# Optimization experiments

Measured on AMD Instinct MI355X. Metric: run time of the kernel, lower is better.

## Reference

```python
import jax, jax.numpy as jnp
import numpy as np

D = 4096; K = 512; HOP = 512; WIN = 16384
NUM_REGIONS = 1 + (WIN - D) // HOP            # 25
D2_Y = 128; K2 = 128; STRIDE_Y = 2
D3_X = 25; K3 = 256
NR2Y = 1 + (K - D2_Y) // STRIDE_Y             # 193
NR3X = 1 + (NUM_REGIONS - D3_X)               # 1
M = 128


def create_filters(d=D, k=K, sr=44100, start_freq=50, end_freq=6000):
    x = jnp.linspace(0.0, 2 * np.pi, d + 1)[:d]
    num_cycles = start_freq * d / sr
    scaling_ind = np.log(end_freq / start_freq) / k
    window_mask = 1.0 - jnp.cos(x)
    phases = jnp.exp(jnp.arange(float(k)) * scaling_ind)[None, :] * num_cycles * x[:, None]
    filters = jnp.stack((jnp.cos(phases), jnp.sin(phases)), axis=2) * window_mask[:, None, None]
    return filters.astype(jnp.float32)          # [d, k, 2]


def setup_inputs() -> dict:
    key = jax.random.key(0)
    k1, k2, k3, k4 = jax.random.split(key, 4)
    x = jax.random.normal(k1, (128, WIN), dtype=jnp.float32)
    filters = create_filters().reshape(D, 2 * K)                     # [4096, 1024]
    # Conv weights in OIHW layout (torch Conv2d convention), kaiming-ish scale
    conv1_w = jax.random.normal(k2, (K2, 1, 1, D2_Y), dtype=jnp.float32) / np.sqrt(D2_Y)
    conv2_w = jax.random.normal(k3, (K3, K2, D3_X, 1), dtype=jnp.float32) / np.sqrt(K2 * D3_X)
    beta_w = jax.random.normal(k4, (M, NR3X * NR2Y * K3), dtype=jnp.float32) / np.sqrt(NR3X * NR2Y * K3)
    return {"x": x, "filters": filters, "conv1_w": conv1_w, "conv2_w": conv2_w, "beta_w": beta_w}


def reference(x, filters, conv1_w, conv2_w, beta_w):
    B = x.shape[0]
    # unfold(1, D, HOP): overlapping windows -> [B, NUM_REGIONS, D]
    idx = jnp.arange(NUM_REGIONS)[:, None] * HOP + jnp.arange(D)[None, :]
    windows = x[:, idx]                                               # [B, 25, 4096]
    spec = windows @ filters                                          # [B, 25, 1024]
    # complex magnitude^2: pairs of (cos, sin) components
    zx = jnp.sum(spec.reshape(B, NUM_REGIONS, K, 2) ** 2, axis=3)     # [B, 25, 512]
    zx = jnp.log(zx + 1e-14)[:, None]                                 # [B, 1, 25, 512]
    dn = ("NCHW", "OIHW", "NCHW")
    h = jax.lax.conv_general_dilated(zx, conv1_w, (1, STRIDE_Y), "VALID", dimension_numbers=dn)
    h = jax.nn.relu(h)                                                # [B, 128, 25, 193]
    h = jax.lax.conv_general_dilated(h, conv2_w, (1, 1), "VALID", dimension_numbers=dn)
    h = jax.nn.relu(h)                                                # [B, 256, 1, 193]
    y = h.reshape(B, -1) @ beta_w.T                                   # [B, 128]
    return y
```

## Files before the change

### kernel.cpp

```cpp
#include <hip/hip_runtime.h>
#include <hip/hip_bf16.h>
#include <math.h>


typedef __attribute__((ext_vector_type(8))) short s8v;
typedef __attribute__((ext_vector_type(8))) _Float16 half8;
typedef __attribute__((ext_vector_type(16))) float f16v;

__device__ inline ushort f2bf(float f) {
    union { float f; unsigned u; } v; v.f = f;
    unsigned u = v.u;
    return (ushort)((u + 0x7FFFu + ((u >> 16) & 1u)) >> 16);
}

#define K0_E0 2097152
#define K0_E1 2621440
#define K0_E2 2637824
#define K0_E3 3457024
#define K0_E4 9781248
__global__ __launch_bounds__(256)
void k0all(const float* __restrict__ x, const float* __restrict__ filt,
           const float* __restrict__ w1, const float* __restrict__ w2,
           const float* __restrict__ beta,
           _Float16* __restrict__ xh, _Float16* __restrict__ fB,
           ushort* __restrict__ w1b, ushort* __restrict__ w2c,
           ushort* __restrict__ bb) {
    for (int i = blockIdx.x * 256 + threadIdx.x; i < K0_E4; i += gridDim.x * 256) {
        if (i < K0_E0) {
            xh[i] = (_Float16)x[i];
        } else if (i < K0_E1) {
            int o = i - K0_E0;
            int kc8 = o >> 10, nn = o & 1023;
            const float* fp = filt + (size_t)(kc8 * 8) * 1024 + nn;
            half8 v;
#pragma unroll
            for (int j = 0; j < 8; j++) v[j] = (_Float16)fp[(size_t)j * 1024];
            *(half8*)(fB + (size_t)o * 8) = v;
        } else if (i < K0_E2) {
            int o = i - K0_E1;
            w1b[o] = f2bf(w1[o]);
        } else if (i < K0_E3) {
            int o = i - K0_E2;
            int k2 = o & 127;
            int dx = (o >> 7) % 25;
            int k3 = o / 3200;
            w2c[o] = f2bf(w2[(k3 * 128 + k2) * 25 + dx]);
        } else {
            int o = i - K0_E3;
            bb[o] = f2bf(beta[o]);
        }
    }
}

#define K1P(KB, LP, VU, VL, RL, RW, DOPREF, DOWRITE)                               \
  {                                                                                \
    asm volatile("s_waitcnt lgkmcnt(0)" ::: "memory");                             \
    __builtin_amdgcn_s_barrier();                                                  \
    asm volatile("" ::: "memory");                                                 \
    if (DOPREF) {                                                                  \
      RL[0] = *(const half8*)(apt + ((KB) + 2) * 32);                              \
      RL[1] = *(const half8*)(apt + ((KB) + 2) * 32 + 16);                         \
      _Pragma("unroll")                                                            \
      for (int s = 0; s < 2; s++) {                                                \
        const _Float16* pBk = pB + ((size_t)((KB) + 2) * 2 + s) * 16384;           \
        VL[s][0] = *(const half8*)(pBk);                                           \
        VL[s][1] = *(const half8*)(pBk + 256);                                     \
      }                                                                            \
    }                                                                              \
    _Pragma("unroll")                                                              \
    for (int s = 0; s < 2; s++) {                                                  \
      half8 a0 = *(const half8*)((const char*)Al + (LP) * 8192 + s * 4096 +        \
                                 (wm + ml) * 32 + qf * 16);                        \
      half8 a1 = *(const half8*)((const char*)Al + (LP) * 8192 + s * 4096 +        \
                                 (wm + 32 + ml) * 32 + qf * 16);                   \
      acc[0][0] = __builtin_amdgcn_mfma_f32_32x32x16_f16(a0, VU[s][0], acc[0][0], 0, 0, 0); \
      acc[0][1] = __builtin_amdgcn_mfma_f32_32x32x16_f16(a0, VU[s][1], acc[0][1], 0, 0, 0); \
      acc[1][0] = __builtin_amdgcn_mfma_f32_32x32x16_f16(a1, VU[s][0], acc[1][0], 0, 0, 0); \
      acc[1][1] = __builtin_amdgcn_mfma_f32_32x32x16_f16(a1, VU[s][1], acc[1][1], 0, 0, 0); \
    }                                                                              \
    if (DOWRITE) {                                                                 \
      half8* dnx = (half8*)((char*)Al + (1 - (LP)) * 8192);                        \
      dnx[t] = RW[0];                                                              \
      dnx[256 + t] = RW[1];                                                        \
    }                                                                              \
  }

__global__ __launch_bounds__(256)
void k1_mfma(const _Float16* __restrict__ xh, const _Float16* __restrict__ fB,
             ushort* __restrict__ zxb) {
    __shared__ _Float16 Al[2][4096];
    const int t  = threadIdx.x;
    const int n0 = blockIdx.y * 128;
    const int m0 = blockIdx.x * 128;
    const int w  = t >> 6, l = t & 63;
    const int wm = (w >> 1) * 64, wn = (w & 1) * 64;
    const int qf = l >> 5;
    const int ml = l & 31;

    const int srow = t >> 1;
    const int sq   = t & 1;
    const int gm   = m0 + srow;
    const _Float16* apt = xh + (gm / 25) * 16384 + (gm % 25) * 512 + sq * 8;

    const _Float16* pB = fB + ((size_t)qf * 1024 + (size_t)(n0 + wn + ml)) * 8;

    f16v acc[2][2];
#pragma unroll
    for (int i = 0; i < 2; i++)
#pragma unroll
        for (int j = 0; j < 2; j++)
#pragma unroll
            for (int r = 0; r < 16; r++) acc[i][j][r] = 0.f;

    half8 vb0[2][2], vb1[2][2], vb2[2][2], vb3[2][2];
    half8 rA0[2], rA1[2];

    {
        rA0[0] = *(const half8*)(apt);
        rA0[1] = *(const half8*)(apt + 16);
        half8* d0 = (half8*)Al;
        d0[t] = rA0[0];
        d0[256 + t] = rA0[1];
        rA1[0] = *(const half8*)(apt + 32);
        rA1[1] = *(const half8*)(apt + 48);
#pragma unroll
        for (int s = 0; s < 2; s++) {
            const _Float16* pBk = pB + (size_t)s * 16384;
            vb0[s][0] = *(const half8*)(pBk);
            vb0[s][1] = *(const half8*)(pBk + 256);
            const _Float16* pBk1 = pB + ((size_t)2 + s) * 16384;
            vb1[s][0] = *(const half8*)(pBk1);
            vb1[s][1] = *(const half8*)(pBk1 + 256);
        }
    }

    for (int it = 0; it < 31; it++) {
        const int kb = it * 4;
        K1P(kb + 0, 0, vb0, vb2, rA0, rA1, true, true)
        K1P(kb + 1, 1, vb1, vb3, rA1, rA0, true, true)
        K1P(kb + 2, 0, vb2, vb0, rA0, rA1, true, true)
        K1P(kb + 3, 1, vb3, vb1, rA1, rA0, true, true)
    }
    K1P(124, 0, vb0, vb2, rA0, rA1, true, true)
    K1P(125, 1, vb1, vb3, rA1, rA0, true, true)
    K1P(126, 0, vb2, vb0, rA0, rA1, false, true)
    K1P(127, 1, vb3, vb1, rA1, rA0, false, false)

#pragma unroll
    for (int mt = 0; mt < 2; mt++)
#pragma unroll
        for (int nt = 0; nt < 2; nt++) {
#pragma unroll
            for (int r = 0; r < 16; r++) {
                float val = acc[mt][nt][r];
                float oth = __shfl_xor(val, 1, 64);
                if (!(l & 1)) {
                    float pw = fmaf(val, val, fmaf(oth, oth, 1e-14f));
                    int m = m0 + wm + mt * 32 + 4 * qf + (r & 3) + 8 * (r >> 2);
                    int n = n0 + wn + nt * 32 + ml;
                    zxb[m * 512 + (n >> 1)] = f2bf(logf(pw));
                }
            }
        }
}

#define ZPITCH 272
__global__ __launch_bounds__(256, 2)
void k2_mfma(const ushort* __restrict__ zxb, const ushort* __restrict__ w1b,
             const ushort* __restrict__ w2c, ushort* __restrict__ h2b) {
    __shared__ ushort zl[2 * 3 * 4 * ZPITCH];
    __shared__ ushort h1l[3 * 16 * 64 * 8];
    const int t  = threadIdx.x;
    const int yt = blockIdx.x;
    const int b  = blockIdx.y;
    const int y0 = yt * 64;
    const int w  = t >> 6;
    const int l  = t & 63;
    const int yy = l & 31;
    const int q  = l >> 5;

    s8v w1f[8];
    {
        const ushort* wp = w1b + (32 * w + yy) * 128 + 8 * q;
#pragma unroll
        for (int ks = 0; ks < 8; ks++)
            w1f[ks] = *(const s8v*)(wp + 16 * ks);
    }

    f16v acc[2][2];
#pragma unroll
    for (int mt = 0; mt < 2; mt++)
#pragma unroll
        for (int nt = 0; nt < 2; nt++)
#pragma unroll
            for (int r = 0; r < 16; r++) acc[mt][nt][r] = 0.f;

    {
        const int nq = 3 * 4 * 62;
        for (int idx = t; idx < nq; idx += 256) {
            int iq = idx % 62;
            int dc = idx / 62;
            int c = dc & 3, d = dc >> 2;
            const ushort* src = zxb + ((b * 25 + d) << 9);
            int gg = 2 * y0 + 2 * c + 4 * iq;
            ushort* dst = zl + (d * 4 + c) * ZPITCH + 4 * iq;
#pragma unroll
            for (int u = 0; u < 4; u++) {
                int g = gg + u;
                dst[u] = (g < 512) ? src[g] : (ushort)0;
            }
        }
    }

    for (int ch = 0; ch < 9; ch++) {
        const int p  = ch & 1;
        const int nd = (ch == 8) ? 1 : 3;
        __syncthreads();

        ushort pv[12];
        int nq2 = 0;
        if (ch < 8) {
            const int nd2 = (ch == 7) ? 1 : 3;
            nq2 = nd2 * 4 * 62;
#pragma unroll
            for (int r = 0; r < 3; r++) {
                int idx = t + r * 256;
                if (idx < nq2) {
                    int iq = idx % 62;
                    int dc = idx / 62;
                    int c = dc & 3, d = dc >> 2;
                    const ushort* src = zxb + ((b * 25 + (ch + 1) * 3 + d) << 9);
                    int gg = 2 * y0 + 2 * c + 4 * iq;
#pragma unroll
                    for (int u = 0; u < 4; u++) {
                        int g = gg + u;
                        pv[r * 4 + u] = (g < 512) ? src[g] : (ushort)0;
                    }
                }
            }
        }

        for (int d = 0; d < nd; d++) {
            const int zb = (p * 3 + d) * 4;
#pragma unroll
            for (int nt = 0; nt < 2; nt++) {
                const int ye = nt * 32 + yy;
                const ushort* zp = zl + (zb + (ye & 3)) * ZPITCH + 8 * (ye >> 2) + 8 * q;
                f16v a1;
#pragma unroll
                for (int r = 0; r < 16; r++) a1[r] = 0.f;
#pragma unroll
                for (int ks = 0; ks < 8; ks++) {
                    s8v bf = *(const s8v*)(zp + 16 * ks);
                    a1 = __builtin_amdgcn_mfma_f32_32x32x16_bf16(w1f[ks], bf, a1, 0, 0, 0);
                }
#pragma unroll
                for (int g = 0; g < 4; g++) {
                    unsigned p0 = (unsigned)f2bf(fmaxf(a1[4 * g + 0], 0.f))
                                | ((unsigned)f2bf(fmaxf(a1[4 * g + 1], 0.f)) << 16);
                    unsigned p1 = (unsigned)f2bf(fmaxf(a1[4 * g + 2], 0.f))
                                | ((unsigned)f2bf(fmaxf(a1[4 * g + 3], 0.f)) << 16);
                    unsigned* dst = (unsigned*)(h1l + (((d * 16 + 4 * w + g) * 64) + ye) * 8 + 4 * q);
                    dst[0] = p0; dst[1] = p1;
                }
            }
        }

        if (ch < 8) {
#pragma unroll
            for (int r = 0; r < 3; r++) {
                int idx = t + r * 256;
                if (idx < nq2) {
                    int iq = idx % 62;
                    int dc = idx / 62;
                    int c = dc & 3, d = dc >> 2;
                    ushort* dst = zl + (((1 - p) * 3 + d) * 4 + c) * ZPITCH + 4 * iq;
#pragma unroll
                    for (int u = 0; u < 4; u++) dst[u] = pv[r * 4 + u];
                }
            }
        }

        __syncthreads();

        for (int d = 0; d < nd; d++) {
            const int dxa = ch * 3 + d;
            const ushort* ap = w2c + (size_t)(64 * w + yy) * 3200 + dxa * 128 + 8 * q;
#pragma unroll
            for (int ks = 0; ks < 8; ks++) {
                s8v a0 = *(const s8v*)(ap + 16 * ks);
                s8v a1f = *(const s8v*)(ap + (size_t)32 * 3200 + 16 * ks);
#pragma unroll
                for (int nt = 0; nt < 2; nt++) {
                    s8v hb = *(const s8v*)(h1l + (((d * 16 + 2 * ks + q) * 64) + nt * 32 + yy) * 8);
                    acc[0][nt] = __builtin_amdgcn_mfma_f32_32x32x16_bf16(a0, hb, acc[0][nt], 0, 0, 0);
                    acc[1][nt] = __builtin_amdgcn_mfma_f32_32x32x16_bf16(a1f, hb, acc[1][nt], 0, 0, 0);
                }
            }
        }
    }

#pragma unroll
    for (int mt = 0; mt < 2; mt++)
#pragma unroll
        for (int nt = 0; nt < 2; nt++) {
            int y = y0 + nt * 32 + yy;
            if (y < 193) {
#pragma unroll
                for (int r = 0; r < 16; r++) {
                    int k3 = 64 * w + 32 * mt + (r & 3) + 8 * (r >> 2) + 4 * q;
                    h2b[(b * 256 + k3) * 193 + y] = f2bf(fmaxf(acc[mt][nt][r], 0.f));
                }
            }
        }
}

__global__ __launch_bounds__(256)
void k4_mfma(const ushort* __restrict__ h2b, const ushort* __restrict__ bb,
             float* __restrict__ part) {
    const int t = threadIdx.x, w = t >> 6, l = t & 63;
    const int s = blockIdx.x;
    const int kb = s * 256;
    const int qf = l >> 5;
    const int ml = l & 31;
    const ushort* pa  = h2b + (size_t)(w * 32 + ml) * 49408 + kb + qf * 8;
    const ushort* pb0 = bb  + (size_t)ml * 49408 + kb + qf * 8;

    f16v acc[4];
#pragma unroll
    for (int nt = 0; nt < 4; nt++)
#pragma unroll
        for (int r = 0; r < 16; r++) acc[nt][r] = 0.f;

    for (int ks = 0; ks < 16; ks++) {
        s8v af = *(const s8v*)(pa + ks * 16);
#pragma unroll
        for (int nt = 0; nt < 4; nt++) {
            s8v bf = *(const s8v*)(pb0 + (size_t)nt * 32 * 49408 + ks * 16);
            acc[nt] = __builtin_amdgcn_mfma_f32_32x32x16_bf16(af, bf, acc[nt], 0, 0, 0);
        }
    }
    float* pp = part + (size_t)s * 16384;
#pragma unroll
    for (int nt = 0; nt < 4; nt++)
#pragma unroll
        for (int r = 0; r < 16; r++) {
            int m = w * 32 + 4 * qf + (r & 3) + 8 * (r >> 2);
            pp[m * 128 + nt * 32 + ml] = acc[nt][r];
        }
}

__global__ __launch_bounds__(256)
void k5_red(const float* __restrict__ part, float* __restrict__ out) {
    __shared__ float red[256];
    const int t  = threadIdx.x;
    const int io = t & 63;
    const int kq = t >> 6;
    const int i  = blockIdx.x * 64 + io;
    float s = 0.f;
#pragma unroll 4
    for (int k = kq; k < 193; k += 4) s += part[(size_t)k * 16384 + i];
    red[t] = s;
    __syncthreads();
    if (t < 64)
        out[blockIdx.x * 64 + t] = (red[t] + red[t + 64]) + (red[t + 128] + red[t + 192]);
}

extern "C" void kernel_launch(void* const* d_in, const int* in_sizes, int n_in,
                              void* d_out, int out_size, void* d_ws, size_t ws_size,
                              hipStream_t stream) {
    const float* x    = (const float*)d_in[0];
    const float* filt = (const float*)d_in[1];
    const float* w1   = (const float*)d_in[2];
    const float* w2   = (const float*)d_in[3];
    const float* beta = (const float*)d_in[4];
    float* out = (float*)d_out;

    char* ws = (char*)d_ws;
    ushort*   zxb  = (ushort*)(ws + 0);
    ushort*   h2b  = (ushort*)(ws + 3276800);
    ushort*   w1b  = (ushort*)(ws + 15921152);
    ushort*   w2c  = (ushort*)(ws + 15953920);
    ushort*   bb   = (ushort*)(ws + 17592320);
    _Float16* xh   = (_Float16*)(ws + 30240768);
    _Float16* fB   = (_Float16*)(ws + 34435072);
    float*    part = (float*)(ws + 30240768);

    k0all<<<2048, 256, 0, stream>>>(x, filt, w1, w2, beta, xh, fB, w1b, w2c, bb);
    k1_mfma<<<dim3(25, 8), 256, 0, stream>>>(xh, fB, zxb);
    k2_mfma<<<dim3(4, 128), 256, 0, stream>>>(zxb, w1b, w2c, h2b);
    k4_mfma<<<193, 256, 0, stream>>>(h2b, bb, part);
    k5_red<<<256, 256, 0, stream>>>(part, out);
}
```

Measured before the change: 284.5 us.

## Load GEMM A fragments directly from global memory, dropping LDS staging

The k1 spectrogram GEMM no longer stages the A (windowed signal) tile through double-buffered LDS with barriers and manual register prefetch. Each wave now reads its A and B fragments straight from global memory in a simple unrolled loop. This removes the per-step barriers and LDS traffic but gives up explicit software pipelining. Each A row is now fetched by both N-waves instead of once per block, so the code leans on L1/L2 hits and compiler scheduling to hide latency.

```diff
diff --git a/kernel.cpp b/kernel.cpp
--- a/kernel.cpp
+++ b/kernel.cpp
@@ -52,57 +52,22 @@
     }
 }
 
-#define K1P(KB, LP, VU, VL, RL, RW, DOPREF, DOWRITE)                               \
-  {                                                                                \
-    asm volatile("s_waitcnt lgkmcnt(0)" ::: "memory");                             \
-    __builtin_amdgcn_s_barrier();                                                  \
-    asm volatile("" ::: "memory");                                                 \
-    if (DOPREF) {                                                                  \
-      RL[0] = *(const half8*)(apt + ((KB) + 2) * 32);                              \
-      RL[1] = *(const half8*)(apt + ((KB) + 2) * 32 + 16);                         \
-      _Pragma("unroll")                                                            \
-      for (int s = 0; s < 2; s++) {                                                \
-        const _Float16* pBk = pB + ((size_t)((KB) + 2) * 2 + s) * 16384;           \
-        VL[s][0] = *(const half8*)(pBk);                                           \
-        VL[s][1] = *(const half8*)(pBk + 256);                                     \
-      }                                                                            \
-    }                                                                              \
-    _Pragma("unroll")                                                              \
-    for (int s = 0; s < 2; s++) {                                                  \
-      half8 a0 = *(const half8*)((const char*)Al + (LP) * 8192 + s * 4096 +        \
-                                 (wm + ml) * 32 + qf * 16);                        \
-      half8 a1 = *(const half8*)((const char*)Al + (LP) * 8192 + s * 4096 +        \
-                                 (wm + 32 + ml) * 32 + qf * 16);                   \
-      acc[0][0] = __builtin_amdgcn_mfma_f32_32x32x16_f16(a0, VU[s][0], acc[0][0], 0, 0, 0); \
-      acc[0][1] = __builtin_amdgcn_mfma_f32_32x32x16_f16(a0, VU[s][1], acc[0][1], 0, 0, 0); \
-      acc[1][0] = __builtin_amdgcn_mfma_f32_32x32x16_f16(a1, VU[s][0], acc[1][0], 0, 0, 0); \
-      acc[1][1] = __builtin_amdgcn_mfma_f32_32x32x16_f16(a1, VU[s][1], acc[1][1], 0, 0, 0); \
-    }                                                                              \
-    if (DOWRITE) {                                                                 \
-      half8* dnx = (half8*)((char*)Al + (1 - (LP)) * 8192);                        \
-      dnx[t] = RW[0];                                                              \
-      dnx[256 + t] = RW[1];                                                        \
-    }                                                                              \
-  }
-
 __global__ __launch_bounds__(256)
 void k1_mfma(const _Float16* __restrict__ xh, const _Float16* __restrict__ fB,
              ushort* __restrict__ zxb) {
-    __shared__ _Float16 Al[2][4096];
     const int t  = threadIdx.x;
+    const int m0 = blockIdx.x * 128;
     const int n0 = blockIdx.y * 128;
-    const int m0 = blockIdx.x * 128;
     const int w  = t >> 6, l = t & 63;
     const int wm = (w >> 1) * 64, wn = (w & 1) * 64;
     const int qf = l >> 5;
     const int ml = l & 31;
 
-    const int srow = t >> 1;
-    const int sq   = t & 1;
-    const int gm   = m0 + srow;
-    const _Float16* apt = xh + (gm / 25) * 16384 + (gm % 25) * 512 + sq * 8;
-
-    const _Float16* pB = fB + ((size_t)qf * 1024 + (size_t)(n0 + wn + ml)) * 8;
+    const int gm0 = m0 + wm + ml;
+    const int gm1 = gm0 + 32;
+    const _Float16* pA0 = xh + (gm0 / 25) * 16384 + (gm0 % 25) * 512 + qf * 8;
+    const _Float16* pA1 = xh + (gm1 / 25) * 16384 + (gm1 % 25) * 512 + qf * 8;
+    const _Float16* pB  = fB + ((size_t)qf * 1024 + (size_t)(n0 + wn + ml)) * 8;
 
     f16v acc[2][2];
 #pragma unroll
@@ -112,39 +77,22 @@
 #pragma unroll
             for (int r = 0; r < 16; r++) acc[i][j][r] = 0.f;
 
-    half8 vb0[2][2], vb1[2][2], vb2[2][2], vb3[2][2];
-    half8 rA0[2], rA1[2];
-
-    {
-        rA0[0] = *(const half8*)(apt);
-        rA0[1] = *(const half8*)(apt + 16);
-        half8* d0 = (half8*)Al;
-        d0[t] = rA0[0];
-        d0[256 + t] = rA0[1];
-        rA1[0] = *(const half8*)(apt + 32);
-        rA1[1] = *(const half8*)(apt + 48);
+#pragma unroll 4
+    for (int kb = 0; kb < 128; kb++) {
 #pragma unroll
         for (int s = 0; s < 2; s++) {
-            const _Float16* pBk = pB + (size_t)s * 16384;
-            vb0[s][0] = *(const half8*)(pBk);
-            vb0[s][1] = *(const half8*)(pBk + 256);
-            const _Float16* pBk1 = pB + ((size_t)2 + s) * 16384;
-            vb1[s][0] = *(const half8*)(pBk1);
-            vb1[s][1] = *(const half8*)(pBk1 + 256);
-        }
-    }
-
-    for (int it = 0; it < 31; it++) {
-        const int kb = it * 4;
-        K1P(kb + 0, 0, vb0, vb2, rA0, rA1, true, true)
-        K1P(kb + 1, 1, vb1, vb3, rA1, rA0, true, true)
-        K1P(kb + 2, 0, vb2, vb0, rA0, rA1, true, true)
-        K1P(kb + 3, 1, vb3, vb1, rA1, rA0, true, true)
-    }
-    K1P(124, 0, vb0, vb2, rA0, rA1, true, true)
-    K1P(125, 1, vb1, vb3, rA1, rA0, true, true)
-    K1P(126, 0, vb2, vb0, rA0, rA1, false, true)
-    K1P(127, 1, vb3, vb1, rA1, rA0, false, false)
+            const int ko = kb * 2 + s;
+            half8 a0 = *(const half8*)(pA0 + ko * 16);
+            half8 a1 = *(const half8*)(pA1 + ko * 16);
+            const _Float16* pBk = pB + (size_t)ko * 16384;
+            half8 b0 = *(const half8*)(pBk);
+            half8 b1 = *(const half8*)(pBk + 256);
+            acc[0][0] = __builtin_amdgcn_mfma_f32_32x32x16_f16(a0, b0, acc[0][0], 0, 0, 0);
+            acc[0][1] = __builtin_amdgcn_mfma_f32_32x32x16_f16(a0, b1, acc[0][1], 0, 0, 0);
+            acc[1][0] = __builtin_amdgcn_mfma_f32_32x32x16_f16(a1, b0, acc[1][0], 0, 0, 0);
+            acc[1][1] = __builtin_amdgcn_mfma_f32_32x32x16_f16(a1, b1, acc[1][1], 0, 0, 0);
+        }
+    }
 
 #pragma unroll
     for (int mt = 0; mt < 2; mt++)
```

Measured after the change: 347.1 us. 22.0% more time.
